# Kernel tuning notes

Measured on AMD Instinct MI355X. Metric: run time of the kernel, lower is better.

Reference implementation:

```python
import jax, jax.numpy as jnp
import numpy as np

B, T, D, H = 2, 2048, 1024, 16
HD = D // H
FF = 4 * D
EPS = 1e-5


def rmsnorm(x, w):
    var = jnp.mean(jnp.square(x), axis=-1, keepdims=True)
    return x * jax.lax.rsqrt(var + EPS) * w


def setup_inputs() -> dict:
    key = jax.random.key(0)
    ks = jax.random.split(key, 17)
    sc = 0.02
    d = {}
    d["x"] = jax.random.normal(ks[0], (B, T, D), jnp.float32)
    d["x_token"] = jax.random.normal(ks[1], (B, T, D), jnp.float32)
    d["pos_emb"] = jax.random.normal(ks[2], (T, D), jnp.float32)
    d["lc_weight"] = jax.random.normal(ks[3], (1,), jnp.float32)
    d["Wq"] = jax.random.normal(ks[4], (D, D), jnp.float32) * sc  # per-head query weights stacked
    d["Wk"] = jax.random.normal(ks[5], (D, D), jnp.float32) * sc
    d["Wv"] = jax.random.normal(ks[6], (D, D), jnp.float32) * sc
    d["proj_w"] = jax.random.normal(ks[7], (D, D), jnp.float32) * sc
    d["proj_b"] = jnp.zeros((D,), jnp.float32)
    d["w1_w"] = jax.random.normal(ks[8], (FF, D), jnp.float32) * sc
    d["w1_b"] = jnp.zeros((FF,), jnp.float32)
    d["w2_w"] = jax.random.normal(ks[9], (D, FF), jnp.float32) * sc
    d["w2_b"] = jnp.zeros((D,), jnp.float32)
    d["w3_w"] = jax.random.normal(ks[10], (FF, D), jnp.float32) * sc
    d["w3_b"] = jnp.zeros((FF,), jnp.float32)
    d["norm1_w"] = jnp.ones((D,), jnp.float32)
    d["norm2_w"] = jnp.ones((D,), jnp.float32)
    return d


def reference(x, x_token, pos_emb, lc_weight, Wq, Wk, Wv, proj_w, proj_b,
              w1_w, w1_b, w2_w, w2_b, w3_w, w3_b, norm1_w, norm2_w):
    lc = jax.nn.sigmoid(lc_weight)  # scalar gate
    x_att = lc * x + (1.0 - lc) * x_token
    xn = rmsnorm(x_att, norm1_w)

    # q, v from normed gated input; k from raw positional embedding (faithful to source)
    q = (xn @ Wq.T).reshape(B, T, H, HD)
    k = (pos_emb @ Wk.T).reshape(T, H, HD)
    v = (xn @ Wv.T).reshape(B, T, H, HD)

    # NOTE: scale uses full model dim E (=D), not head_size, as in the source
    scores = jnp.einsum('bqhd,khd->bhqk', q, k) * (D ** -0.5)
    causal = jnp.tril(jnp.ones((T, T), bool))
    scores = jnp.where(causal, scores, -jnp.inf)
    p = jax.nn.softmax(scores, axis=-1)
    attn = jnp.einsum('bhqk,bkhd->bqhd', p, v).reshape(B, T, D)

    x = x + attn @ proj_w.T + proj_b

    xn2 = rmsnorm(x, norm2_w)
    h = jax.nn.silu(xn2 @ w1_w.T + w1_b) * (xn2 @ w3_w.T + w3_b)
    return x + h @ w2_w.T + w2_b
```

## Files before the change

kernel.cpp:

```cpp
#include <hip/hip_runtime.h>
#include <hip/hip_bf16.h>


typedef __hip_bfloat16 bf16;
typedef __attribute__((ext_vector_type(8))) short bf16x8;
typedef __attribute__((ext_vector_type(4))) float floatx4;

constexpr int cB = 2, cT = 2048, cD = 1024, cH = 16, cFF = 4096;
constexpr float cEPS = 1e-5f;
constexpr unsigned BF16_ONES = 0x3F803F80u;

__device__ __forceinline__ float b2f(bf16 x) { return __bfloat162float(x); }
__device__ __forceinline__ bf16  f2b(float x) { return __float2bfloat16(x); }
__device__ __forceinline__ unsigned short f2bu(float x) {
  bf16 t = __float2bfloat16(x);
  union { bf16 b; unsigned short u; } cv;
  cv.b = t;
  return cv.u;
}
__device__ __forceinline__ float loadR(const bf16* p)  { return b2f(*p); }
__device__ __forceinline__ float loadR(const float* p) { return *p; }

__device__ __forceinline__ void gload16(const bf16* g, unsigned short* l) {
  __builtin_amdgcn_global_load_lds(
      (const __attribute__((address_space(1))) void*)g,
      (__attribute__((address_space(3))) void*)l, 16, 0, 0);
}

struct ConvArgs {
  const void* src[17];
  bf16* dst[17];
  int n[17];
  int sb[17];
};

__global__ __launch_bounds__(256) void convert_all_k(ConvArgs a) {
  const int bid = blockIdx.x;
  int seg = 0;
#pragma unroll
  for (int i = 1; i < 17; i++) seg = (bid >= a.sb[i]) ? i : seg;
  const int n = a.n[seg];
  const int i0 = (bid - a.sb[seg]) * 2048 + threadIdx.x * 8;
  if (i0 >= n) return;
  const bool isb = (((const unsigned*)a.src[15])[0] == BF16_ONES);
  const void* src = a.src[seg];
  bf16* dst = a.dst[seg];
  if (i0 + 8 <= n) {
    if (isb) {
      *(int4*)(dst + i0) = *(const int4*)((const bf16*)src + i0);
    } else {
      float4 f0 = *(const float4*)((const float*)src + i0);
      float4 f1 = *(const float4*)((const float*)src + i0 + 4);
      int4 ro;
      bf16* po = (bf16*)&ro;
      po[0] = f2b(f0.x); po[1] = f2b(f0.y); po[2] = f2b(f0.z); po[3] = f2b(f0.w);
      po[4] = f2b(f1.x); po[5] = f2b(f1.y); po[6] = f2b(f1.z); po[7] = f2b(f1.w);
      *(int4*)(dst + i0) = ro;
    }
  } else {
    for (int j = i0; j < n; j++)
      dst[j] = isb ? ((const bf16*)src)[j] : f2b(((const float*)src)[j]);
  }
}

template <int TN, int OUTK, typename ResT>
__device__ __forceinline__ void gemm_core(
    const bf16* __restrict__ A, const bf16* __restrict__ W,
    const bf16* __restrict__ bias, const ResT* __restrict__ R,
    void* __restrict__ Cv, const unsigned* __restrict__ dbits,
    int crow0, int N, int K, int m0, int n0,
    unsigned short* As, unsigned short* Bs)
{
  constexpr int NTN = TN / 32;
  const int tid  = threadIdx.x;
  const int wave = tid >> 6;
  const int lane = tid & 63;
  const int l15  = lane & 15;
  const int quad = lane >> 4;
  const int wm   = (wave >> 1) * 64;
  const int wn   = (wave & 1) * (TN / 2);

  bool obf = (OUTK != 1);
  if (OUTK == 2) obf = (*dbits == BF16_ONES);

  const int lr  = lane >> 2;
  const int lc8 = (lane & 3) * 8;
  const bf16* Ag0 = A + (size_t)(m0 + wave * 32 + lr) * K + lc8;
  const bf16* Ag1 = Ag0 + (size_t)16 * K;
  unsigned short* lA0 = &As[(wave * 32) * 32];
  unsigned short* lA1 = &As[(wave * 32 + 16) * 32];
  const bf16* Bg0 = W + (size_t)(n0 + wave * (TN / 4) + lr) * K + lc8;
  const bf16* Bg1 = Bg0 + (size_t)16 * K;
  unsigned short* lB0 = &Bs[(wave * (TN / 4)) * 32];
  unsigned short* lB1 = &Bs[(wave * (TN / 4) + 16) * 32];

  floatx4 acc[4][NTN];
#pragma unroll
  for (int i = 0; i < 4; i++)
#pragma unroll
    for (int j = 0; j < NTN; j++) acc[i][j] = (floatx4){0.f, 0.f, 0.f, 0.f};

  for (int k0 = 0; k0 < K; k0 += 32) {
    gload16(Ag0 + k0, lA0);
    gload16(Ag1 + k0, lA1);
    gload16(Bg0 + k0, lB0);
    if (TN == 128) gload16(Bg1 + k0, lB1);
    __syncthreads();

    bf16x8 a[4], b[NTN];
#pragma unroll
    for (int t = 0; t < 4; t++)
      a[t] = *(const bf16x8*)&As[(wm + t * 16 + l15) * 32 + quad * 8];
#pragma unroll
    for (int t = 0; t < NTN; t++)
      b[t] = *(const bf16x8*)&Bs[(wn + t * 16 + l15) * 32 + quad * 8];
#pragma unroll
    for (int tm = 0; tm < 4; tm++)
#pragma unroll
      for (int tn = 0; tn < NTN; tn++)
        acc[tm][tn] = __builtin_amdgcn_mfma_f32_16x16x32_bf16(a[tm], b[tn], acc[tm][tn], 0, 0, 0);
    __syncthreads();
  }

#pragma unroll
  for (int tm = 0; tm < 4; tm++) {
#pragma unroll
    for (int tn = 0; tn < NTN; tn++) {
      const int row = m0 + wm + tm * 16 + quad * 4;
      const int col = n0 + wn + tn * 16 + l15;
      float bv = bias ? b2f(bias[col]) : 0.f;
#pragma unroll
      for (int i = 0; i < 4; i++) {
        float val = acc[tm][tn][i] + bv;
        const size_t ridx = (size_t)(row + i) * N + col;
        const size_t cidx = (size_t)(crow0 + row + i) * N + col;
        if (R) val += loadR(&R[ridx]);
        if (OUTK == 0)      ((bf16*)Cv)[cidx] = f2b(val);
        else if (OUTK == 1) ((float*)Cv)[cidx] = val;
        else { if (obf) ((bf16*)Cv)[cidx] = f2b(val); else ((float*)Cv)[cidx] = val; }
      }
    }
  }
}

template <int TN, int OUTK, typename ResT>
__global__ __launch_bounds__(256) void gemm_t(
    const bf16* __restrict__ A, const bf16* __restrict__ W,
    const bf16* __restrict__ bias, const ResT* __restrict__ R,
    void* __restrict__ Cv, const unsigned* __restrict__ dbits,
    int crow0, int M, int N, int K)
{
  __shared__ __align__(16) unsigned short As[128 * 32];
  __shared__ __align__(16) unsigned short Bs[TN * 32];
  gemm_core<TN, OUTK, ResT>(A, W, bias, R, Cv, dbits, crow0, N, K,
                            blockIdx.y * 128, blockIdx.x * TN, As, Bs);
}

__global__ __launch_bounds__(256) void gemm_qkv(
    const bf16* __restrict__ xn, const bf16* __restrict__ pos,
    const bf16* __restrict__ Wq, const bf16* __restrict__ Wv,
    const bf16* __restrict__ Wk,
    bf16* __restrict__ q, bf16* __restrict__ v, bf16* __restrict__ kb)
{
  const int z = blockIdx.z;
  if (z == 2 && blockIdx.y >= 16) return;
  __shared__ __align__(16) unsigned short As[128 * 32];
  __shared__ __align__(16) unsigned short Bs[64 * 32];
  const bf16* A = (z == 2) ? pos : xn;
  const bf16* W = (z == 0) ? Wq : (z == 1) ? Wv : Wk;
  bf16* C = (z == 0) ? q : (z == 1) ? v : kb;
  gemm_core<64, 0, bf16>(A, W, nullptr, (const bf16*)nullptr, C, nullptr, 0,
                         cD, cD, blockIdx.y * 128, blockIdx.x * 64, As, Bs);
}

__global__ __launch_bounds__(256, 2) void gemm_w13(
    const bf16* __restrict__ A,
    const bf16* __restrict__ W1, const bf16* __restrict__ b1,
    const bf16* __restrict__ W3, const bf16* __restrict__ b3,
    bf16* __restrict__ H, int N, int K)
{
  __shared__ __align__(16) unsigned short As[128 * 32];
  __shared__ __align__(16) unsigned short B1s[128 * 32];
  __shared__ __align__(16) unsigned short B3s[128 * 32];
  const int tid  = threadIdx.x;
  const int m0   = blockIdx.y * 128;
  const int n0   = blockIdx.x * 128;
  const int wave = tid >> 6;
  const int lane = tid & 63;
  const int l15  = lane & 15;
  const int quad = lane >> 4;
  const int wm   = (wave >> 1) * 64;
  const int wn   = (wave & 1) * 64;

  const int lr  = lane >> 2;
  const int lc8 = (lane & 3) * 8;
  const bf16* Ag0  = A  + (size_t)(m0 + wave * 32 + lr) * K + lc8;
  const bf16* Ag1  = Ag0 + (size_t)16 * K;
  const bf16* B1g0 = W1 + (size_t)(n0 + wave * 32 + lr) * K + lc8;
  const bf16* B1g1 = B1g0 + (size_t)16 * K;
  const bf16* B3g0 = W3 + (size_t)(n0 + wave * 32 + lr) * K + lc8;
  const bf16* B3g1 = B3g0 + (size_t)16 * K;
  unsigned short* lA0 = &As[(wave * 32) * 32];
  unsigned short* lA1 = &As[(wave * 32 + 16) * 32];
  unsigned short* l10 = &B1s[(wave * 32) * 32];
  unsigned short* l11 = &B1s[(wave * 32 + 16) * 32];
  unsigned short* l30 = &B3s[(wave * 32) * 32];
  unsigned short* l31 = &B3s[(wave * 32 + 16) * 32];

  floatx4 acc1[4][4], acc3[4][4];
#pragma unroll
  for (int i = 0; i < 4; i++)
#pragma unroll
    for (int j = 0; j < 4; j++) {
      acc1[i][j] = (floatx4){0.f, 0.f, 0.f, 0.f};
      acc3[i][j] = (floatx4){0.f, 0.f, 0.f, 0.f};
    }

  for (int k0 = 0; k0 < K; k0 += 32) {
    gload16(Ag0 + k0, lA0);
    gload16(Ag1 + k0, lA1);
    gload16(B1g0 + k0, l10);
    gload16(B1g1 + k0, l11);
    gload16(B3g0 + k0, l30);
    gload16(B3g1 + k0, l31);
    __syncthreads();

    bf16x8 a[4], v1[4], v3[4];
#pragma unroll
    for (int t = 0; t < 4; t++) {
      a[t]  = *(const bf16x8*)&As[(wm + t * 16 + l15) * 32 + quad * 8];
      v1[t] = *(const bf16x8*)&B1s[(wn + t * 16 + l15) * 32 + quad * 8];
      v3[t] = *(const bf16x8*)&B3s[(wn + t * 16 + l15) * 32 + quad * 8];
    }
#pragma unroll
    for (int tm = 0; tm < 4; tm++)
#pragma unroll
      for (int tn = 0; tn < 4; tn++) {
        acc1[tm][tn] = __builtin_amdgcn_mfma_f32_16x16x32_bf16(a[tm], v1[tn], acc1[tm][tn], 0, 0, 0);
        acc3[tm][tn] = __builtin_amdgcn_mfma_f32_16x16x32_bf16(a[tm], v3[tn], acc3[tm][tn], 0, 0, 0);
      }
    __syncthreads();
  }

#pragma unroll
  for (int tm = 0; tm < 4; tm++) {
#pragma unroll
    for (int tn = 0; tn < 4; tn++) {
      const int row = m0 + wm + tm * 16 + quad * 4;
      const int col = n0 + wn + tn * 16 + l15;
      const float bv1 = b2f(b1[col]);
      const float bv3 = b2f(b3[col]);
#pragma unroll
      for (int i = 0; i < 4; i++) {
        float g = acc1[tm][tn][i] + bv1;
        float u = acc3[tm][tn][i] + bv3;
        float val = g * (1.f / (1.f + __expf(-g))) * u;
        H[(size_t)(row + i) * N + col] = f2b(val);
      }
    }
  }
}

template <bool GATE, typename InT>
__global__ __launch_bounds__(256) void rmsnorm_k(
    const InT* __restrict__ X, const bf16* __restrict__ XT,
    const bf16* __restrict__ LC, const bf16* __restrict__ Wn,
    bf16* __restrict__ O)
{
  const int row = blockIdx.x;
  const int tid = threadIdx.x;
  const size_t base = (size_t)row * cD;
  const int c = tid * 4;

  float lc = 1.f, lc1 = 0.f;
  if (GATE) {
    float g = b2f(LC[0]);
    lc = 1.f / (1.f + __expf(-g));
    lc1 = 1.f - lc;
  }

  float xv[4];
  if (sizeof(InT) == 2) {
    ushort4 u = *(const ushort4*)((const unsigned short*)X + base + c);
    const bf16* pu = (const bf16*)&u;
#pragma unroll
    for (int i = 0; i < 4; i++) xv[i] = b2f(pu[i]);
  } else {
    float4 f = *(const float4*)((const float*)X + base + c);
    xv[0] = f.x; xv[1] = f.y; xv[2] = f.z; xv[3] = f.w;
  }
  if (GATE) {
    ushort4 u = *(const ushort4*)((const unsigned short*)XT + base + c);
    const bf16* pu = (const bf16*)&u;
#pragma unroll
    for (int i = 0; i < 4; i++) xv[i] = lc * xv[i] + lc1 * b2f(pu[i]);
  }

  float ss = xv[0] * xv[0] + xv[1] * xv[1] + xv[2] * xv[2] + xv[3] * xv[3];
#pragma unroll
  for (int off = 32; off; off >>= 1) ss += __shfl_xor(ss, off, 64);

  __shared__ float red[4];
  if ((tid & 63) == 0) red[tid >> 6] = ss;
  __syncthreads();
  float tot = red[0] + red[1] + red[2] + red[3];
  float rs = rsqrtf(tot * (1.f / cD) + cEPS);

  ushort4 o;
  bf16* po = (bf16*)&o;
#pragma unroll
  for (int i = 0; i < 4; i++) po[i] = f2b(xv[i] * rs * b2f(Wn[c + i]));
  *(ushort4*)((unsigned short*)O + base + c) = o;
}

__global__ __launch_bounds__(256) void fattn_k(
    const bf16* __restrict__ Q, const bf16* __restrict__ K,
    const bf16* __restrict__ V, bf16* __restrict__ O)
{
  constexpr int LQ = 72, LK = 72, LV = 72;
  __shared__ __align__(16) unsigned short Qs[128 * LQ];
  __shared__ __align__(16) unsigned short Ks[64 * LK];
  __shared__ __align__(16) unsigned short Vs[64 * LV];

  const int tid  = threadIdx.x;
  const int wave = tid >> 6;
  const int lane = tid & 63;
  const int l15  = lane & 15;
  const int quad = lane >> 4;
  const int blk  = blockIdx.x;
  const int qt   = 15 - (blk & 15);
  const int h    = (blk >> 4) & 15;
  const int b    = blk >> 8;
  const int q0   = qt * 128;

  const bf16* Qb = Q + ((size_t)b * cT) * cD + h * 64;
  const bf16* Kb = K + h * 64;
  const bf16* Vb = V + ((size_t)b * cT) * cD + h * 64;

  {
    const int qr = tid >> 1, qc = (tid & 1) * 32;
    const bf16* gq = Qb + (size_t)(q0 + qr) * cD + qc;
    *(int4*)&Qs[qr * LQ + qc]      = *(const int4*)(gq);
    *(int4*)&Qs[qr * LQ + qc + 8]  = *(const int4*)(gq + 8);
    *(int4*)&Qs[qr * LQ + qc + 16] = *(const int4*)(gq + 16);
    *(int4*)&Qs[qr * LQ + qc + 24] = *(const int4*)(gq + 24);
  }
  __syncthreads();

  const int qw = wave * 32;
  bf16x8 qa[2][2];
#pragma unroll
  for (int mt = 0; mt < 2; mt++)
#pragma unroll
    for (int dc = 0; dc < 2; dc++)
      qa[mt][dc] = *(const bf16x8*)&Qs[(qw + mt * 16 + l15) * LQ + dc * 32 + quad * 8];

  float l_i[2][4];
  floatx4 oacc[2][4];
#pragma unroll
  for (int mt = 0; mt < 2; mt++) {
#pragma unroll
    for (int i = 0; i < 4; i++) l_i[mt][i] = 0.f;
#pragma unroll
    for (int dt = 0; dt < 4; dt++) oacc[mt][dt] = (floatx4){0.f, 0.f, 0.f, 0.f};
  }

  const int ktiles = 2 * qt + 2;
  const int qend_w = q0 + qw + 32;
  unsigned short* Pw = &Qs[qw * LQ];

  const int kr = tid >> 2, kc = (tid & 3) * 16;
  int4 kpre0, kpre1;
  unsigned short vpre[16];
  {
    const bf16* g = Kb + (size_t)kr * cD + kc;
    kpre0 = *(const int4*)g;
    kpre1 = *(const int4*)(g + 8);
    const unsigned short* gv = (const unsigned short*)(Vb + (size_t)(wave * 16) * cD + lane);
#pragma unroll
    for (int j = 0; j < 16; j++) vpre[j] = gv[(size_t)j * cD];
  }

  for (int it = 0; it < ktiles; ++it) {
    const int k0 = it * 64;
    __syncthreads();
    *(int4*)&Ks[kr * LK + kc]     = kpre0;
    *(int4*)&Ks[kr * LK + kc + 8] = kpre1;
    {
      union { unsigned short us[8]; int4 v4; } pk0, pk1;
#pragma unroll
      for (int j = 0; j < 8; j++) { pk0.us[j] = vpre[j]; pk1.us[j] = vpre[8 + j]; }
      *(int4*)&Vs[lane * LV + wave * 16]     = pk0.v4;
      *(int4*)&Vs[lane * LV + wave * 16 + 8] = pk1.v4;
    }
    __syncthreads();

    if (it + 1 < ktiles) {
      const bf16* g = Kb + (size_t)(k0 + 64 + kr) * cD + kc;
      kpre0 = *(const int4*)g;
      kpre1 = *(const int4*)(g + 8);
      const unsigned short* gv = (const unsigned short*)(Vb + (size_t)(k0 + 64 + wave * 16) * cD + lane);
#pragma unroll
      for (int j = 0; j < 16; j++) vpre[j] = gv[(size_t)j * cD];
    }

    if (k0 < qend_w) {
      floatx4 s[2][4];
#pragma unroll
      for (int st = 0; st < 4; st++) {
        bf16x8 kb0 = *(const bf16x8*)&Ks[(st * 16 + l15) * LK + quad * 8];
        bf16x8 kb1 = *(const bf16x8*)&Ks[(st * 16 + l15) * LK + 32 + quad * 8];
#pragma unroll
        for (int mt = 0; mt < 2; mt++) {
          s[mt][st] = (floatx4){0.f, 0.f, 0.f, 0.f};
          s[mt][st] = __builtin_amdgcn_mfma_f32_16x16x32_bf16(qa[mt][0], kb0, s[mt][st], 0, 0, 0);
          s[mt][st] = __builtin_amdgcn_mfma_f32_16x16x32_bf16(qa[mt][1], kb1, s[mt][st], 0, 0, 0);
        }
      }
      float p[2][4][4];
#pragma unroll
      for (int mt = 0; mt < 2; mt++)
#pragma unroll
        for (int i = 0; i < 4; i++) {
          const int qrow = q0 + qw + mt * 16 + quad * 4 + i;
          float rs = 0.f;
#pragma unroll
          for (int st = 0; st < 4; st++) {
            const int kp = k0 + st * 16 + l15;
            float pv = (kp > qrow) ? 0.f : __expf(s[mt][st][i] * 0.03125f);
            p[mt][st][i] = pv;
            rs += pv;
          }
#pragma unroll
          for (int off = 1; off < 16; off <<= 1) rs += __shfl_xor(rs, off, 64);
          l_i[mt][i] += rs;
        }
#pragma unroll
      for (int mt = 0; mt < 2; mt++)
#pragma unroll
        for (int st = 0; st < 4; st++)
#pragma unroll
          for (int i = 0; i < 4; i++)
            Pw[(mt * 16 + quad * 4 + i) * LQ + st * 16 + l15] = f2bu(p[mt][st][i]);
      bf16x8 pa[2][2];
#pragma unroll
      for (int mt = 0; mt < 2; mt++)
#pragma unroll
        for (int pc = 0; pc < 2; pc++)
          pa[mt][pc] = *(const bf16x8*)&Pw[(mt * 16 + l15) * LQ + pc * 32 + quad * 8];
#pragma unroll
      for (int dt = 0; dt < 4; dt++) {
        bf16x8 vb0 = *(const bf16x8*)&Vs[(dt * 16 + l15) * LV + quad * 8];
        bf16x8 vb1 = *(const bf16x8*)&Vs[(dt * 16 + l15) * LV + 32 + quad * 8];
#pragma unroll
        for (int mt = 0; mt < 2; mt++) {
          oacc[mt][dt] = __builtin_amdgcn_mfma_f32_16x16x32_bf16(pa[mt][0], vb0, oacc[mt][dt], 0, 0, 0);
          oacc[mt][dt] = __builtin_amdgcn_mfma_f32_16x16x32_bf16(pa[mt][1], vb1, oacc[mt][dt], 0, 0, 0);
        }
      }
    }
  }

#pragma unroll
  for (int mt = 0; mt < 2; mt++) {
    float rl[4];
#pragma unroll
    for (int i = 0; i < 4; i++) rl[i] = 1.f / l_i[mt][i];
    const size_t obase = ((size_t)b * cT + q0 + qw + mt * 16) * cD + h * 64;
#pragma unroll
    for (int dt = 0; dt < 4; dt++)
#pragma unroll
      for (int i = 0; i < 4; i++)
        O[obase + (size_t)(quad * 4 + i) * cD + dt * 16 + l15] = f2b(oacc[mt][dt][i] * rl[i]);
  }
}

extern "C" void kernel_launch(void* const* d_in, const int* in_sizes, int n_in,
                              void* d_out, int out_size, void* d_ws, size_t ws_size,
                              hipStream_t stream) {
  char* ws = (char*)d_ws;
  const size_t MB = 1u << 20;
  const int BT = cB * cT;

  bf16* cxt  = (bf16*)(ws + 0);
  bf16* cpos = (bf16*)(ws + 8 * MB);
  bf16* q    = (bf16*)(ws + 12 * MB);
  bf16* kbuf = (bf16*)(ws + 20 * MB);
  bf16* v    = (bf16*)(ws + 24 * MB);
  bf16* h    = (bf16*)(ws + 0);
  size_t off = 32 * MB;
  auto alloc = [&](size_t bytes) -> char* {
    char* p = ws + off;
    off = (off + bytes + 255) & ~(size_t)255;
    return p;
  };
  bf16*  cx  = (bf16*)alloc((size_t)BT * cD * 2);
  bf16*  xn  = (bf16*)alloc((size_t)BT * cD * 2);
  float* x2  = (float*)alloc((size_t)BT * cD * 4);
  bf16*  xn2 = (bf16*)alloc((size_t)BT * cD * 2);
  bf16* cin[17];
  cin[0] = cx; cin[1] = cxt; cin[2] = cpos;
  for (int i = 3; i < 17; i++) cin[i] = (bf16*)alloc((size_t)in_sizes[i] * 2);

  const unsigned* dbits = (const unsigned*)d_in[15];
  dim3 blk(256);

  ConvArgs ca;
  int nblk = 0;
  for (int i = 0; i < 17; i++) {
    ca.src[i] = d_in[i];
    ca.dst[i] = cin[i];
    ca.n[i] = in_sizes[i];
    ca.sb[i] = nblk;
    nblk += (in_sizes[i] + 2047) / 2048;
  }
  convert_all_k<<<nblk, blk, 0, stream>>>(ca);

  const bf16 *clc = cin[3], *cWq = cin[4], *cWk = cin[5], *cWv = cin[6];
  const bf16 *cprojw = cin[7], *cprojb = cin[8];
  const bf16 *cw1w = cin[9], *cw1b = cin[10], *cw2w = cin[11], *cw2b = cin[12];
  const bf16 *cw3w = cin[13], *cw3b = cin[14], *cn1 = cin[15], *cn2 = cin[16];

  rmsnorm_k<true, bf16><<<BT, blk, 0, stream>>>(cx, cxt, clc, cn1, xn);
  gemm_qkv<<<dim3(cD / 64, BT / 128, 3), blk, 0, stream>>>(
      xn, cpos, cWq, cWv, cWk, q, v, kbuf);
  bf16* attn = xn;
  fattn_k<<<cB * cH * (cT / 128), blk, 0, stream>>>(q, kbuf, v, attn);
  gemm_t<64, 1, bf16><<<dim3(cD / 64, BT / 128), blk, 0, stream>>>(
      attn, cprojw, cprojb, cx, x2, nullptr, 0, BT, cD, cD);
  rmsnorm_k<false, float><<<BT, blk, 0, stream>>>(
      x2, (const bf16*)nullptr, (const bf16*)nullptr, cn2, xn2);
  gemm_w13<<<dim3(cFF / 128, BT / 128), blk, 0, stream>>>(
      xn2, cw1w, cw1b, cw3w, cw3b, h, cFF, cD);
  gemm_t<64, 2, float><<<dim3(cD / 64, BT / 128), blk, 0, stream>>>(
      h, cw2w, cw2b, x2, d_out, dbits, 0, BT, cD, cFF);
  (void)n_in; (void)out_size; (void)ws_size;
}
```

Baseline: 487.3 us.

## Shrink attention query tile to 64 rows and defer row-sum reductions

The flash-attention kernel now handles 64 query rows per block (16 per wave) instead of 128, doubling the grid to 1024 blocks and halving shared memory for Q. Per-row softmax denominators are kept as per-lane partial sums and reduced across lanes once at the end, replacing a shuffle reduction on every key tile. The aim is better occupancy and load balance across the causal triangle, plus fewer shuffles. The cost is twice as many loads of each K/V tile per query row, since each block reuses K/V across fewer queries.

```diff
diff --git a/kernel.cpp b/kernel.cpp
--- a/kernel.cpp
+++ b/kernel.cpp
@@ -318,7 +318,7 @@
     const bf16* __restrict__ V, bf16* __restrict__ O)
 {
   constexpr int LQ = 72, LK = 72, LV = 72;
-  __shared__ __align__(16) unsigned short Qs[128 * LQ];
+  __shared__ __align__(16) unsigned short Qs[64 * LQ];
   __shared__ __align__(16) unsigned short Ks[64 * LK];
   __shared__ __align__(16) unsigned short Vs[64 * LV];
 
@@ -328,45 +328,35 @@
   const int l15  = lane & 15;
   const int quad = lane >> 4;
   const int blk  = blockIdx.x;
-  const int qt   = 15 - (blk & 15);
-  const int h    = (blk >> 4) & 15;
-  const int b    = blk >> 8;
-  const int q0   = qt * 128;
+  const int qt   = 31 - (blk & 31);
+  const int h    = (blk >> 5) & 15;
+  const int b    = blk >> 9;
+  const int q0   = qt * 64;
 
   const bf16* Qb = Q + ((size_t)b * cT) * cD + h * 64;
   const bf16* Kb = K + h * 64;
   const bf16* Vb = V + ((size_t)b * cT) * cD + h * 64;
 
   {
-    const int qr = tid >> 1, qc = (tid & 1) * 32;
+    const int qr = tid >> 2, qc = (tid & 3) * 16;
     const bf16* gq = Qb + (size_t)(q0 + qr) * cD + qc;
-    *(int4*)&Qs[qr * LQ + qc]      = *(const int4*)(gq);
-    *(int4*)&Qs[qr * LQ + qc + 8]  = *(const int4*)(gq + 8);
-    *(int4*)&Qs[qr * LQ + qc + 16] = *(const int4*)(gq + 16);
-    *(int4*)&Qs[qr * LQ + qc + 24] = *(const int4*)(gq + 24);
+    *(int4*)&Qs[qr * LQ + qc]     = *(const int4*)(gq);
+    *(int4*)&Qs[qr * LQ + qc + 8] = *(const int4*)(gq + 8);
   }
   __syncthreads();
 
-  const int qw = wave * 32;
-  bf16x8 qa[2][2];
-#pragma unroll
-  for (int mt = 0; mt < 2; mt++)
-#pragma unroll
-    for (int dc = 0; dc < 2; dc++)
-      qa[mt][dc] = *(const bf16x8*)&Qs[(qw + mt * 16 + l15) * LQ + dc * 32 + quad * 8];
-
-  float l_i[2][4];
-  floatx4 oacc[2][4];
-#pragma unroll
-  for (int mt = 0; mt < 2; mt++) {
-#pragma unroll
-    for (int i = 0; i < 4; i++) l_i[mt][i] = 0.f;
-#pragma unroll
-    for (int dt = 0; dt < 4; dt++) oacc[mt][dt] = (floatx4){0.f, 0.f, 0.f, 0.f};
-  }
-
-  const int ktiles = 2 * qt + 2;
-  const int qend_w = q0 + qw + 32;
+  const int qw = wave * 16;
+  bf16x8 qa[2];
+#pragma unroll
+  for (int dc = 0; dc < 2; dc++)
+    qa[dc] = *(const bf16x8*)&Qs[(qw + l15) * LQ + dc * 32 + quad * 8];
+
+  float l_p[4] = {0.f, 0.f, 0.f, 0.f};
+  floatx4 oacc[4];
+#pragma unroll
+  for (int dt = 0; dt < 4; dt++) oacc[dt] = (floatx4){0.f, 0.f, 0.f, 0.f};
+
+  const int ktiles = qt + 1;
   unsigned short* Pw = &Qs[qw * LQ];
 
   const int kr = tid >> 2, kc = (tid & 3) * 16;
@@ -404,75 +394,59 @@
       for (int j = 0; j < 16; j++) vpre[j] = gv[(size_t)j * cD];
     }
 
-    if (k0 < qend_w) {
-      floatx4 s[2][4];
+    floatx4 s[4];
+#pragma unroll
+    for (int st = 0; st < 4; st++) {
+      bf16x8 kb0 = *(const bf16x8*)&Ks[(st * 16 + l15) * LK + quad * 8];
+      bf16x8 kb1 = *(const bf16x8*)&Ks[(st * 16 + l15) * LK + 32 + quad * 8];
+      s[st] = (floatx4){0.f, 0.f, 0.f, 0.f};
+      s[st] = __builtin_amdgcn_mfma_f32_16x16x32_bf16(qa[0], kb0, s[st], 0, 0, 0);
+      s[st] = __builtin_amdgcn_mfma_f32_16x16x32_bf16(qa[1], kb1, s[st], 0, 0, 0);
+    }
+    float p[4][4];
+#pragma unroll
+    for (int i = 0; i < 4; i++) {
+      const int qrow = q0 + qw + quad * 4 + i;
 #pragma unroll
       for (int st = 0; st < 4; st++) {
-        bf16x8 kb0 = *(const bf16x8*)&Ks[(st * 16 + l15) * LK + quad * 8];
-        bf16x8 kb1 = *(const bf16x8*)&Ks[(st * 16 + l15) * LK + 32 + quad * 8];
-#pragma unroll
-        for (int mt = 0; mt < 2; mt++) {
-          s[mt][st] = (floatx4){0.f, 0.f, 0.f, 0.f};
-          s[mt][st] = __builtin_amdgcn_mfma_f32_16x16x32_bf16(qa[mt][0], kb0, s[mt][st], 0, 0, 0);
-          s[mt][st] = __builtin_amdgcn_mfma_f32_16x16x32_bf16(qa[mt][1], kb1, s[mt][st], 0, 0, 0);
-        }
+        const int kp = k0 + st * 16 + l15;
+        float pv = (kp > qrow) ? 0.f : __expf(s[st][i] * 0.03125f);
+        p[st][i] = pv;
+        l_p[i] += pv;
       }
-      float p[2][4][4];
-#pragma unroll
-      for (int mt = 0; mt < 2; mt++)
-#pragma unroll
-        for (int i = 0; i < 4; i++) {
-          const int qrow = q0 + qw + mt * 16 + quad * 4 + i;
-          float rs = 0.f;
-#pragma unroll
-          for (int st = 0; st < 4; st++) {
-            const int kp = k0 + st * 16 + l15;
-            float pv = (kp > qrow) ? 0.f : __expf(s[mt][st][i] * 0.03125f);
-            p[mt][st][i] = pv;
-            rs += pv;
-          }
-#pragma unroll
-          for (int off = 1; off < 16; off <<= 1) rs += __shfl_xor(rs, off, 64);
-          l_i[mt][i] += rs;
-        }
-#pragma unroll
-      for (int mt = 0; mt < 2; mt++)
-#pragma unroll
-        for (int st = 0; st < 4; st++)
-#pragma unroll
-          for (int i = 0; i < 4; i++)
-            Pw[(mt * 16 + quad * 4 + i) * LQ + st * 16 + l15] = f2bu(p[mt][st][i]);
-      bf16x8 pa[2][2];
-#pragma unroll
-      for (int mt = 0; mt < 2; mt++)
-#pragma unroll
-        for (int pc = 0; pc < 2; pc++)
-          pa[mt][pc] = *(const bf16x8*)&Pw[(mt * 16 + l15) * LQ + pc * 32 + quad * 8];
-#pragma unroll
-      for (int dt = 0; dt < 4; dt++) {
-        bf16x8 vb0 = *(const bf16x8*)&Vs[(dt * 16 + l15) * LV + quad * 8];
-        bf16x8 vb1 = *(const bf16x8*)&Vs[(dt * 16 + l15) * LV + 32 + quad * 8];
-#pragma unroll
-        for (int mt = 0; mt < 2; mt++) {
-          oacc[mt][dt] = __builtin_amdgcn_mfma_f32_16x16x32_bf16(pa[mt][0], vb0, oacc[mt][dt], 0, 0, 0);
-          oacc[mt][dt] = __builtin_amdgcn_mfma_f32_16x16x32_bf16(pa[mt][1], vb1, oacc[mt][dt], 0, 0, 0);
-        }
-      }
-    }
-  }
-
-#pragma unroll
-  for (int mt = 0; mt < 2; mt++) {
-    float rl[4];
-#pragma unroll
-    for (int i = 0; i < 4; i++) rl[i] = 1.f / l_i[mt][i];
-    const size_t obase = ((size_t)b * cT + q0 + qw + mt * 16) * cD + h * 64;
-#pragma unroll
-    for (int dt = 0; dt < 4; dt++)
+    }
+#pragma unroll
+    for (int st = 0; st < 4; st++)
 #pragma unroll
       for (int i = 0; i < 4; i++)
-        O[obase + (size_t)(quad * 4 + i) * cD + dt * 16 + l15] = f2b(oacc[mt][dt][i] * rl[i]);
-  }
+        Pw[(quad * 4 + i) * LQ + st * 16 + l15] = f2bu(p[st][i]);
+    bf16x8 pa[2];
+#pragma unroll
+    for (int pc = 0; pc < 2; pc++)
+      pa[pc] = *(const bf16x8*)&Pw[l15 * LQ + pc * 32 + quad * 8];
+#pragma unroll
+    for (int dt = 0; dt < 4; dt++) {
+      bf16x8 vb0 = *(const bf16x8*)&Vs[(dt * 16 + l15) * LV + quad * 8];
+      bf16x8 vb1 = *(const bf16x8*)&Vs[(dt * 16 + l15) * LV + 32 + quad * 8];
+      oacc[dt] = __builtin_amdgcn_mfma_f32_16x16x32_bf16(pa[0], vb0, oacc[dt], 0, 0, 0);
+      oacc[dt] = __builtin_amdgcn_mfma_f32_16x16x32_bf16(pa[1], vb1, oacc[dt], 0, 0, 0);
+    }
+  }
+
+  float rl[4];
+#pragma unroll
+  for (int i = 0; i < 4; i++) {
+    float li = l_p[i];
+#pragma unroll
+    for (int off = 1; off < 16; off <<= 1) li += __shfl_xor(li, off, 64);
+    rl[i] = 1.f / li;
+  }
+  const size_t obase = ((size_t)b * cT + q0 + qw) * cD + h * 64;
+#pragma unroll
+  for (int dt = 0; dt < 4; dt++)
+#pragma unroll
+    for (int i = 0; i < 4; i++)
+      O[obase + (size_t)(quad * 4 + i) * cD + dt * 16 + l15] = f2b(oacc[dt][i] * rl[i]);
 }
 
 extern "C" void kernel_launch(void* const* d_in, const int* in_sizes, int n_in,
@@ -525,7 +499,7 @@
   gemm_qkv<<<dim3(cD / 64, BT / 128, 3), blk, 0, stream>>>(
       xn, cpos, cWq, cWv, cWk, q, v, kbuf);
   bf16* attn = xn;
-  fattn_k<<<cB * cH * (cT / 128), blk, 0, stream>>>(q, kbuf, v, attn);
+  fattn_k<<<cB * cH * (cT / 64), blk, 0, stream>>>(q, kbuf, v, attn);
   gemm_t<64, 1, bf16><<<dim3(cD / 64, BT / 128), blk, 0, stream>>>(
       attn, cprojw, cprojb, cx, x2, nullptr, 0, BT, cD, cD);
   rmsnorm_k<false, float><<<BT, blk, 0, stream>>>(
```

New measurement: 481.0 us. Within noise of the previous version (-1.3%).
